# Kernel tuning notes

Measured on AMD Instinct MI355X. Metric: run time of the kernel, lower is better.

## Reference

```python
import jax, jax.numpy as jnp
import numpy as np

HIDDEN = 512

def setup_inputs() -> dict:
    key = jax.random.key(0)
    ks = jax.random.split(key, 6)
    B, T = 65536, 100
    scale = 0.1  # keep tanh MLP in a sane dynamic range
    return {
        "y0": jax.random.normal(ks[0], (B, 2), jnp.float32),
        "t_points": jnp.arange(T, dtype=jnp.float32) * 0.01,
        "W1": jax.random.normal(ks[1], (2, HIDDEN), jnp.float32) * scale,
        "b1": jnp.zeros((HIDDEN,), jnp.float32),
        "W2": jax.random.normal(ks[2], (HIDDEN, HIDDEN), jnp.float32) * scale,
        "b2": jnp.zeros((HIDDEN,), jnp.float32),
        "W3": jax.random.normal(ks[3], (HIDDEN, HIDDEN // 2), jnp.float32) * scale,
        "b3": jnp.zeros((HIDDEN // 2,), jnp.float32),
        "W4": jax.random.normal(ks[4], (HIDDEN // 2, 2), jnp.float32) * scale,
        "b4": jnp.zeros((2,), jnp.float32),
    }

def _mlp(y, W1, b1, W2, b2, W3, b3, W4, b4):
    # 4-layer tanh MLP: 2 -> H -> H -> H//2 -> 2 (t is unused in ODEFunc)
    h = jnp.tanh(y @ W1 + b1)
    h = jnp.tanh(h @ W2 + b2)
    h = jnp.tanh(h @ W3 + b3)
    return h @ W4 + b4

def reference(y0, t_points, W1, b1, W2, b2, W3, b3, W4, b4):
    f = lambda y: _mlp(y, W1, b1, W2, b2, W3, b3, W4, b4)
    dts = t_points[1:] - t_points[:-1]  # [T-1]

    def step(y, dt):
        k1 = f(y)
        k2 = f(y + k1 * (dt * 0.5))
        k3 = f(y + k2 * (dt * 0.5))
        k4 = f(y + k3 * dt)
        y_next = y + (dt / 6.0) * (k1 + 2.0 * k2 + 2.0 * k3 + k4)
        return y_next, y_next

    _, traj = jax.lax.scan(step, y0, dts)
    return jnp.concatenate([y0[None], traj], axis=0)  # [T, B, 2]
```

## Files before the change

### kernel.cpp

```cpp
#include <hip/hip_runtime.h>
#include <hip/hip_bf16.h>
#include <stdint.h>

using bfrag_t = __attribute__((ext_vector_type(8))) short;
using f32x16  = __attribute__((ext_vector_type(16))) float;

#define HID  512
#define H3   256
#define RB   128
#define NTH  512
#define KSC  2.885390081777927f

static __device__ __forceinline__ uint32_t bf16_rne(float f) {
    uint32_t u = __float_as_uint(f);
    return (u + 0x7fffu + ((u >> 16) & 1u)) >> 16;
}
static __device__ __forceinline__ uint32_t pk_bf16(float a, float b) {
    union { __hip_bfloat162 h; uint32_t u; } c;
    c.h = __float22bfloat162_rn(make_float2(a, b));
    return c.u;
}
static __device__ __forceinline__ float fast_exp2(float x) {
#if __has_builtin(__builtin_amdgcn_exp2f)
    return __builtin_amdgcn_exp2f(x);
#else
    return exp2f(x);
#endif
}
static __device__ __forceinline__ float fast_rcp(float x) {
#if __has_builtin(__builtin_amdgcn_rcpf)
    return __builtin_amdgcn_rcpf(x);
#else
    return 1.0f / x;
#endif
}
static __device__ __forceinline__ float ftanh_s(float xs) {
    float e = fast_exp2(xs);
    return 1.0f - 2.0f * fast_rcp(e + 1.0f);
}
static __device__ __forceinline__ bfrag_t frag_of(uint4 v) {
    union { uint4 u; bfrag_t f; } c; c.u = v; return c.f;
}

__global__ void prep_weights(const float* __restrict__ W1, const float* __restrict__ b1,
                             const float* __restrict__ W2, const float* __restrict__ b2,
                             const float* __restrict__ W3, const float* __restrict__ b3,
                             uint4* __restrict__ o2, uint4* __restrict__ o3,
                             float* __restrict__ w1p, float* __restrict__ b2s,
                             float* __restrict__ b3s)
{
    int id = blockIdx.x * 256 + threadIdx.x;
    if (id < 32768) {
        int l = id & 63, kt = (id >> 6) & 31, mt = id >> 11;
        int m = mt * 32 + (l & 31), k0 = kt * 16 + (l >> 5) * 8;
        uint32_t p[4];
        #pragma unroll
        for (int jj = 0; jj < 4; ++jj) {
            float v0 = KSC * W2[(k0 + jj * 2    ) * 512 + m];
            float v1 = KSC * W2[(k0 + jj * 2 + 1) * 512 + m];
            p[jj] = bf16_rne(v0) | (bf16_rne(v1) << 16);
        }
        o2[id] = make_uint4(p[0], p[1], p[2], p[3]);
    } else if (id < 49152) {
        int id2 = id - 32768;
        int l = id2 & 63, kt = (id2 >> 6) & 31, mt = id2 >> 11;
        int m = mt * 32 + (l & 31), k0 = kt * 16 + (l >> 5) * 8;
        uint32_t p[4];
        #pragma unroll
        for (int jj = 0; jj < 4; ++jj) {
            float v0 = KSC * W3[(k0 + jj * 2    ) * 256 + m];
            float v1 = KSC * W3[(k0 + jj * 2 + 1) * 256 + m];
            p[jj] = bf16_rne(v0) | (bf16_rne(v1) << 16);
        }
        o3[id2] = make_uint4(p[0], p[1], p[2], p[3]);
    } else if (id < 49152 + 1536) {
        int t = id - 49152;
        int ck = t / 24, j = t % 24;
        int f = ck * 8 + (j & 7);
        float v = (j < 8) ? W1[f] : (j < 16) ? W1[512 + f] : b1[f];
        w1p[t] = KSC * v;
    } else if (id < 49152 + 1536 + 512) {
        int i = id - 49152 - 1536; b2s[i] = KSC * b2[i];
    } else if (id < 49152 + 1536 + 512 + 256) {
        int i = id - 49152 - 1536 - 512; b3s[i] = KSC * b3[i];
    }
}

struct SmemT {
    uint4  hbuf[64 * RB];
    float  b2[HID];
    float  b3[H3];
    float  y [RB][2];
    float  z [RB][2];
    float  ya[RB][2];
    float  part[4][RB][2];
};

__global__ __launch_bounds__(NTH, 2) void node_kernel(
    const float* __restrict__ y0, const float* __restrict__ tp,
    const float* __restrict__ W4g, const float* __restrict__ b4g,
    const uint4* __restrict__ w2A, const uint4* __restrict__ w3A,
    const float* __restrict__ w1p, const float* __restrict__ b2s,
    const float* __restrict__ b3s,
    float* __restrict__ out, int Bn, int T)
{
    __shared__ SmemT s;
    const int tid = threadIdx.x;
    const int l   = tid & 63;
    const int w   = tid >> 6;
    const int wu  = __builtin_amdgcn_readfirstlane(w);
    const int b0  = blockIdx.x * RB;
    const int ln  = l & 31, lh = l >> 5;

    for (int i = tid; i < HID; i += NTH) s.b2[i] = b2s[i];
    for (int i = tid; i < H3;  i += NTH) s.b3[i] = b3s[i];
    if (tid < RB) {
        float2 v = ((const float2*)y0)[b0 + tid];
        s.y [tid][0] = v.x; s.y [tid][1] = v.y;
        s.z [tid][0] = v.x; s.z [tid][1] = v.y;
        s.ya[tid][0] = v.x; s.ya[tid][1] = v.y;
        ((float2*)out)[b0 + tid] = v;
    }
    __syncthreads();

    const float* w1w = w1p + wu * 8 * 24;
    const uint4* pW2 = w2A + (wu * 64) * 64 + l;
    const int mg = wu >> 1, ng = wu & 1;
    const uint4* pW3 = w3A + (mg * 64) * 64 + l;

    for (int st = 0; st < T - 1; ++st) {
        float dt = tp[st + 1] - tp[st];

        for (int e = 0; e < 4; ++e) {
            uint4 aC[2], aN[2];
            aC[0] = pW2[0];           aC[1] = pW2[32 * 64];
            aN[0] = pW2[64];          aN[1] = pW2[32 * 64 + 64];

            {
                float zl0 = s.z[l][0],      zl1 = s.z[l][1];
                float zh0 = s.z[64 + l][0], zh1 = s.z[64 + l][1];
                #pragma unroll
                for (int i = 0; i < 8; ++i) {
                    const float* P = w1w + i * 24;
                    int ck = wu * 8 + i;
                    float xa[8], xb[8];
                    #pragma unroll
                    for (int jj = 0; jj < 8; ++jj) {
                        float wa = P[jj], wb = P[8 + jj], bb = P[16 + jj];
                        xa[jj] = ftanh_s(fmaf(zl0, wa, fmaf(zl1, wb, bb)));
                        xb[jj] = ftanh_s(fmaf(zh0, wa, fmaf(zh1, wb, bb)));
                    }
                    s.hbuf[ck * RB + l] = make_uint4(
                        pk_bf16(xa[0], xa[1]), pk_bf16(xa[2], xa[3]),
                        pk_bf16(xa[4], xa[5]), pk_bf16(xa[6], xa[7]));
                    s.hbuf[ck * RB + 64 + l] = make_uint4(
                        pk_bf16(xb[0], xb[1]), pk_bf16(xb[2], xb[3]),
                        pk_bf16(xb[4], xb[5]), pk_bf16(xb[6], xb[7]));
                }
            }
            __syncthreads();

            uint4 a3C[2], a3N[2];
            {
                f32x16 acc[2][4];
                #pragma unroll
                for (int mt = 0; mt < 2; ++mt) {
                    int mb = (wu * 2 + mt) * 32 + 4 * lh;
                    float bv[16];
                    *(float4*)&bv[0]  = *(const float4*)&s.b2[mb];
                    *(float4*)&bv[4]  = *(const float4*)&s.b2[mb + 8];
                    *(float4*)&bv[8]  = *(const float4*)&s.b2[mb + 16];
                    *(float4*)&bv[12] = *(const float4*)&s.b2[mb + 24];
                    f32x16 a;
                    #pragma unroll
                    for (int r = 0; r < 16; ++r) a[r] = bv[r];
                    #pragma unroll
                    for (int nt = 0; nt < 4; ++nt) acc[mt][nt] = a;
                }
                #pragma unroll 2
                for (int kt = 0; kt < 32; ++kt) {
                    uint4 bF[4];
                    #pragma unroll
                    for (int nt = 0; nt < 4; ++nt)
                        bF[nt] = s.hbuf[(kt * 2 + lh) * RB + nt * 32 + ln];
                    int kq = (kt < 30) ? (kt + 2) : 29;
                    uint4 aM0 = pW2[kq * 64];
                    uint4 aM1 = pW2[32 * 64 + kq * 64];
                    #pragma unroll
                    for (int mt = 0; mt < 2; ++mt)
                        #pragma unroll
                        for (int nt = 0; nt < 4; ++nt)
                            acc[mt][nt] = __builtin_amdgcn_mfma_f32_32x32x16_bf16(
                                frag_of(aC[mt]), frag_of(bF[nt]), acc[mt][nt], 0, 0, 0);
                    aC[0] = aN[0]; aC[1] = aN[1];
                    aN[0] = aM0;   aN[1] = aM1;
                }
                a3C[0] = pW3[0];      a3C[1] = pW3[32 * 64];
                a3N[0] = pW3[64];     a3N[1] = pW3[32 * 64 + 64];
                __syncthreads();
                #pragma unroll
                for (int mt = 0; mt < 2; ++mt) {
                    int m0 = (wu * 2 + mt) * 32 + 4 * lh;
                    int hi = lh;
                    #pragma unroll
                    for (int nt = 0; nt < 4; ++nt) {
                        int n = nt * 32 + ln;
                        f32x16 c = acc[mt][nt];
                        #pragma unroll
                        for (int g = 0; g < 4; ++g) {
                            int ck = (m0 + 8 * g) >> 3;
                            uint32_t u0 = pk_bf16(ftanh_s(c[4 * g    ]), ftanh_s(c[4 * g + 1]));
                            uint32_t u1 = pk_bf16(ftanh_s(c[4 * g + 2]), ftanh_s(c[4 * g + 3]));
                            ((uint2*)s.hbuf)[((ck * RB + n) << 1) | hi] = make_uint2(u0, u1);
                        }
                    }
                }
                __syncthreads();
            }

            {
                f32x16 acc[2][2];
                #pragma unroll
                for (int mt = 0; mt < 2; ++mt) {
                    int mb = (mg * 2 + mt) * 32 + 4 * lh;
                    float bv[16];
                    *(float4*)&bv[0]  = *(const float4*)&s.b3[mb];
                    *(float4*)&bv[4]  = *(const float4*)&s.b3[mb + 8];
                    *(float4*)&bv[8]  = *(const float4*)&s.b3[mb + 16];
                    *(float4*)&bv[12] = *(const float4*)&s.b3[mb + 24];
                    f32x16 a;
                    #pragma unroll
                    for (int r = 0; r < 16; ++r) a[r] = bv[r];
                    #pragma unroll
                    for (int nt = 0; nt < 2; ++nt) acc[mt][nt] = a;
                }
                #pragma unroll 2
                for (int kt = 0; kt < 32; ++kt) {
                    uint4 bF[2];
                    #pragma unroll
                    for (int nt = 0; nt < 2; ++nt)
                        bF[nt] = s.hbuf[(kt * 2 + lh) * RB + (ng * 2 + nt) * 32 + ln];
                    int kq = (kt < 30) ? (kt + 2) : 29;
                    uint4 aM0 = pW3[kq * 64];
                    uint4 aM1 = pW3[32 * 64 + kq * 64];
                    #pragma unroll
                    for (int mt = 0; mt < 2; ++mt)
                        #pragma unroll
                        for (int nt = 0; nt < 2; ++nt)
                            acc[mt][nt] = __builtin_amdgcn_mfma_f32_32x32x16_bf16(
                                frag_of(a3C[mt]), frag_of(bF[nt]), acc[mt][nt], 0, 0, 0);
                    a3C[0] = a3N[0]; a3C[1] = a3N[1];
                    a3N[0] = aM0;    a3N[1] = aM1;
                }
                __syncthreads();
                #pragma unroll
                for (int mt = 0; mt < 2; ++mt) {
                    int m0 = (mg * 2 + mt) * 32 + 4 * lh;
                    int hi = lh;
                    #pragma unroll
                    for (int nt = 0; nt < 2; ++nt) {
                        int n = (ng * 2 + nt) * 32 + ln;
                        f32x16 c = acc[mt][nt];
                        #pragma unroll
                        for (int g = 0; g < 4; ++g) {
                            int ck = (m0 + 8 * g) >> 3;
                            uint32_t u0 = pk_bf16(ftanh_s(c[4 * g    ]), ftanh_s(c[4 * g + 1]));
                            uint32_t u1 = pk_bf16(ftanh_s(c[4 * g + 2]), ftanh_s(c[4 * g + 3]));
                            ((uint2*)s.hbuf)[((ck * RB + n) << 1) | hi] = make_uint2(u0, u1);
                        }
                    }
                }
                __syncthreads();
            }

            {
                int r  = tid & 127;
                int qq = __builtin_amdgcn_readfirstlane(tid >> 7);
                float a0 = 0.f, a1 = 0.f;
                #pragma unroll
                for (int j = 0; j < 8; ++j) {
                    int ck = qq * 8 + j;
                    uint4 hv = s.hbuf[ck * RB + r];
                    const uint32_t* pu = (const uint32_t*)&hv;
                    #pragma unroll
                    for (int jj = 0; jj < 4; ++jj) {
                        uint32_t uu = pu[jj];
                        float h0 = __uint_as_float(uu << 16);
                        float h1 = __uint_as_float(uu & 0xffff0000u);
                        int f = ck * 8 + jj * 2;
                        a0 = fmaf(h0, W4g[f * 2],     fmaf(h1, W4g[f * 2 + 2], a0));
                        a1 = fmaf(h0, W4g[f * 2 + 1], fmaf(h1, W4g[f * 2 + 3], a1));
                    }
                }
                s.part[qq][r][0] = a0; s.part[qq][r][1] = a1;
            }
            __syncthreads();

            if (tid < RB) {
                float k0 = s.part[0][tid][0] + s.part[1][tid][0]
                         + s.part[2][tid][0] + s.part[3][tid][0] + b4g[0];
                float k1 = s.part[0][tid][1] + s.part[1][tid][1]
                         + s.part[2][tid][1] + s.part[3][tid][1] + b4g[1];
                float wg = (e == 0 || e == 3) ? dt * (1.f / 6.f) : dt * (1.f / 3.f);
                float ya0 = s.ya[tid][0] + wg * k0;
                float ya1 = s.ya[tid][1] + wg * k1;
                s.ya[tid][0] = ya0; s.ya[tid][1] = ya1;
                if (e < 3) {
                    float aa = (e == 2) ? dt : dt * 0.5f;
                    s.z[tid][0] = s.y[tid][0] + aa * k0;
                    s.z[tid][1] = s.y[tid][1] + aa * k1;
                } else {
                    s.y[tid][0] = ya0; s.y[tid][1] = ya1;
                    s.z[tid][0] = ya0; s.z[tid][1] = ya1;
                    ((float2*)out)[(size_t)(st + 1) * Bn + b0 + tid] =
                        make_float2(ya0, ya1);
                }
            }
            __syncthreads();
        }
    }
}

extern "C" void kernel_launch(void* const* d_in, const int* in_sizes, int n_in,
                              void* d_out, int out_size, void* d_ws, size_t ws_size,
                              hipStream_t stream)
{
    const float* y0 = (const float*)d_in[0];
    const float* tp = (const float*)d_in[1];
    const float* W1 = (const float*)d_in[2];
    const float* b1 = (const float*)d_in[3];
    const float* W2 = (const float*)d_in[4];
    const float* b2 = (const float*)d_in[5];
    const float* W3 = (const float*)d_in[6];
    const float* b3 = (const float*)d_in[7];
    const float* W4 = (const float*)d_in[8];
    const float* b4 = (const float*)d_in[9];
    float* out = (float*)d_out;

    const int Bn = in_sizes[0] / 2;
    const int T  = in_sizes[1];

    uint4* w2A = (uint4*)d_ws;
    uint4* w3A = w2A + 32768;
    float* w1p = (float*)(w3A + 16384);
    float* b2s = w1p + 1536;
    float* b3s = b2s + 512;

    prep_weights<<<201, 256, 0, stream>>>(W1, b1, W2, b2, W3, b3,
                                          w2A, w3A, w1p, b2s, b3s);
    node_kernel<<<Bn / RB, NTH, 0, stream>>>(y0, tp, W4, b4,
                                             w2A, w3A, w1p, b2s, b3s, out, Bn, T);
}
```

Baseline: 21.86 ms.

## Halve rows per block and remap layer-3 warps to single M tiles

Each block now handles 64 batch rows instead of 128, so the grid doubles, and the launch bound asks for 4 blocks per CU instead of 2. Layer 3 is remapped so each warp owns one 32-row M tile across all N columns instead of a 2x2 M/N split. The W4 reduction is spread over 8 partial sums. The goal is more resident blocks to hide latency, but each block now reuses every global W2/W3 fragment over half as many rows, which doubles weight traffic. The tighter register budget and the 64KB-per-block LDS tile may spill registers or leave occupancy unchanged.

```diff
diff --git a/kernel.cpp b/kernel.cpp
--- a/kernel.cpp
+++ b/kernel.cpp
@@ -7,7 +7,7 @@
 
 #define HID  512
 #define H3   256
-#define RB   128
+#define RB   64
 #define NTH  512
 #define KSC  2.885390081777927f
 
@@ -93,10 +93,10 @@
     float  y [RB][2];
     float  z [RB][2];
     float  ya[RB][2];
-    float  part[4][RB][2];
+    float  part[8][RB][2];
 };
 
-__global__ __launch_bounds__(NTH, 2) void node_kernel(
+__global__ __launch_bounds__(NTH, 4) void node_kernel(
     const float* __restrict__ y0, const float* __restrict__ tp,
     const float* __restrict__ W4g, const float* __restrict__ b4g,
     const uint4* __restrict__ w2A, const uint4* __restrict__ w3A,
@@ -125,8 +125,7 @@
 
     const float* w1w = w1p + wu * 8 * 24;
     const uint4* pW2 = w2A + (wu * 64) * 64 + l;
-    const int mg = wu >> 1, ng = wu & 1;
-    const uint4* pW3 = w3A + (mg * 64) * 64 + l;
+    const uint4* pW3 = w3A + (wu * 32) * 64 + l;
 
     for (int st = 0; st < T - 1; ++st) {
         float dt = tp[st + 1] - tp[st];
@@ -137,32 +136,27 @@
             aN[0] = pW2[64];          aN[1] = pW2[32 * 64 + 64];
 
             {
-                float zl0 = s.z[l][0],      zl1 = s.z[l][1];
-                float zh0 = s.z[64 + l][0], zh1 = s.z[64 + l][1];
+                float zl0 = s.z[l][0], zl1 = s.z[l][1];
                 #pragma unroll
                 for (int i = 0; i < 8; ++i) {
                     const float* P = w1w + i * 24;
                     int ck = wu * 8 + i;
-                    float xa[8], xb[8];
+                    float xa[8];
                     #pragma unroll
                     for (int jj = 0; jj < 8; ++jj) {
                         float wa = P[jj], wb = P[8 + jj], bb = P[16 + jj];
                         xa[jj] = ftanh_s(fmaf(zl0, wa, fmaf(zl1, wb, bb)));
-                        xb[jj] = ftanh_s(fmaf(zh0, wa, fmaf(zh1, wb, bb)));
                     }
                     s.hbuf[ck * RB + l] = make_uint4(
                         pk_bf16(xa[0], xa[1]), pk_bf16(xa[2], xa[3]),
                         pk_bf16(xa[4], xa[5]), pk_bf16(xa[6], xa[7]));
-                    s.hbuf[ck * RB + 64 + l] = make_uint4(
-                        pk_bf16(xb[0], xb[1]), pk_bf16(xb[2], xb[3]),
-                        pk_bf16(xb[4], xb[5]), pk_bf16(xb[6], xb[7]));
                 }
             }
             __syncthreads();
 
-            uint4 a3C[2], a3N[2];
+            uint4 a3C, a3N;
             {
-                f32x16 acc[2][4];
+                f32x16 acc[2][2];
                 #pragma unroll
                 for (int mt = 0; mt < 2; ++mt) {
                     int mb = (wu * 2 + mt) * 32 + 4 * lh;
@@ -175,13 +169,13 @@
                     #pragma unroll
                     for (int r = 0; r < 16; ++r) a[r] = bv[r];
                     #pragma unroll
-                    for (int nt = 0; nt < 4; ++nt) acc[mt][nt] = a;
+                    for (int nt = 0; nt < 2; ++nt) acc[mt][nt] = a;
                 }
                 #pragma unroll 2
                 for (int kt = 0; kt < 32; ++kt) {
-                    uint4 bF[4];
-                    #pragma unroll
-                    for (int nt = 0; nt < 4; ++nt)
+                    uint4 bF[2];
+                    #pragma unroll
+                    for (int nt = 0; nt < 2; ++nt)
                         bF[nt] = s.hbuf[(kt * 2 + lh) * RB + nt * 32 + ln];
                     int kq = (kt < 30) ? (kt + 2) : 29;
                     uint4 aM0 = pW2[kq * 64];
@@ -189,21 +183,20 @@
                     #pragma unroll
                     for (int mt = 0; mt < 2; ++mt)
                         #pragma unroll
-                        for (int nt = 0; nt < 4; ++nt)
+                        for (int nt = 0; nt < 2; ++nt)
                             acc[mt][nt] = __builtin_amdgcn_mfma_f32_32x32x16_bf16(
                                 frag_of(aC[mt]), frag_of(bF[nt]), acc[mt][nt], 0, 0, 0);
                     aC[0] = aN[0]; aC[1] = aN[1];
                     aN[0] = aM0;   aN[1] = aM1;
                 }
-                a3C[0] = pW3[0];      a3C[1] = pW3[32 * 64];
-                a3N[0] = pW3[64];     a3N[1] = pW3[32 * 64 + 64];
+                a3C = pW3[0];      a3N = pW3[64];
                 __syncthreads();
                 #pragma unroll
                 for (int mt = 0; mt < 2; ++mt) {
                     int m0 = (wu * 2 + mt) * 32 + 4 * lh;
                     int hi = lh;
                     #pragma unroll
-                    for (int nt = 0; nt < 4; ++nt) {
+                    for (int nt = 0; nt < 2; ++nt) {
                         int n = nt * 32 + ln;
                         f32x16 c = acc[mt][nt];
                         #pragma unroll
@@ -219,10 +212,9 @@
             }
 
             {
-                f32x16 acc[2][2];
-                #pragma unroll
-                for (int mt = 0; mt < 2; ++mt) {
-                    int mb = (mg * 2 + mt) * 32 + 4 * lh;
+                f32x16 acc3[2];
+                {
+                    int mb = wu * 32 + 4 * lh;
                     float bv[16];
                     *(float4*)&bv[0]  = *(const float4*)&s.b3[mb];
                     *(float4*)&bv[4]  = *(const float4*)&s.b3[mb + 8];
@@ -231,36 +223,30 @@
                     f32x16 a;
                     #pragma unroll
                     for (int r = 0; r < 16; ++r) a[r] = bv[r];
-                    #pragma unroll
-                    for (int nt = 0; nt < 2; ++nt) acc[mt][nt] = a;
+                    acc3[0] = a; acc3[1] = a;
                 }
                 #pragma unroll 2
                 for (int kt = 0; kt < 32; ++kt) {
                     uint4 bF[2];
                     #pragma unroll
                     for (int nt = 0; nt < 2; ++nt)
-                        bF[nt] = s.hbuf[(kt * 2 + lh) * RB + (ng * 2 + nt) * 32 + ln];
+                        bF[nt] = s.hbuf[(kt * 2 + lh) * RB + nt * 32 + ln];
                     int kq = (kt < 30) ? (kt + 2) : 29;
-                    uint4 aM0 = pW3[kq * 64];
-                    uint4 aM1 = pW3[32 * 64 + kq * 64];
-                    #pragma unroll
-                    for (int mt = 0; mt < 2; ++mt)
-                        #pragma unroll
-                        for (int nt = 0; nt < 2; ++nt)
-                            acc[mt][nt] = __builtin_amdgcn_mfma_f32_32x32x16_bf16(
-                                frag_of(a3C[mt]), frag_of(bF[nt]), acc[mt][nt], 0, 0, 0);
-                    a3C[0] = a3N[0]; a3C[1] = a3N[1];
-                    a3N[0] = aM0;    a3N[1] = aM1;
+                    uint4 aM = pW3[kq * 64];
+                    #pragma unroll
+                    for (int nt = 0; nt < 2; ++nt)
+                        acc3[nt] = __builtin_amdgcn_mfma_f32_32x32x16_bf16(
+                            frag_of(a3C), frag_of(bF[nt]), acc3[nt], 0, 0, 0);
+                    a3C = a3N; a3N = aM;
                 }
                 __syncthreads();
-                #pragma unroll
-                for (int mt = 0; mt < 2; ++mt) {
-                    int m0 = (mg * 2 + mt) * 32 + 4 * lh;
+                {
+                    int m0 = wu * 32 + 4 * lh;
                     int hi = lh;
                     #pragma unroll
                     for (int nt = 0; nt < 2; ++nt) {
-                        int n = (ng * 2 + nt) * 32 + ln;
-                        f32x16 c = acc[mt][nt];
+                        int n = nt * 32 + ln;
+                        f32x16 c = acc3[nt];
                         #pragma unroll
                         for (int g = 0; g < 4; ++g) {
                             int ck = (m0 + 8 * g) >> 3;
@@ -274,12 +260,12 @@
             }
 
             {
-                int r  = tid & 127;
-                int qq = __builtin_amdgcn_readfirstlane(tid >> 7);
+                int r  = l;
+                int qq = wu;
                 float a0 = 0.f, a1 = 0.f;
                 #pragma unroll
-                for (int j = 0; j < 8; ++j) {
-                    int ck = qq * 8 + j;
+                for (int j = 0; j < 4; ++j) {
+                    int ck = qq * 4 + j;
                     uint4 hv = s.hbuf[ck * RB + r];
                     const uint32_t* pu = (const uint32_t*)&hv;
                     #pragma unroll
@@ -297,10 +283,12 @@
             __syncthreads();
 
             if (tid < RB) {
-                float k0 = s.part[0][tid][0] + s.part[1][tid][0]
-                         + s.part[2][tid][0] + s.part[3][tid][0] + b4g[0];
-                float k1 = s.part[0][tid][1] + s.part[1][tid][1]
-                         + s.part[2][tid][1] + s.part[3][tid][1] + b4g[1];
+                float k0 = b4g[0], k1 = b4g[1];
+                #pragma unroll
+                for (int p = 0; p < 8; ++p) {
+                    k0 += s.part[p][tid][0];
+                    k1 += s.part[p][tid][1];
+                }
                 float wg = (e == 0 || e == 3) ? dt * (1.f / 6.f) : dt * (1.f / 3.f);
                 float ya0 = s.ya[tid][0] + wg * k0;
                 float ya1 = s.ya[tid][1] + wg * k1;
```

Measured after the change: 26.77 ms. 1.22x slower.

## Fuse layer-4 projection into layer-3 MFMA epilogue, drop hbuf round trip

Applied to the files above, without the earlier changes.

The final 256->2 projection is now computed directly from the layer-3 MFMA accumulators in registers, using a W4 copy permuted to the accumulator layout in the prep kernel. Per-wave partial sums go to an 8-way partial buffer that is reduced per row. This removes the bf16 tanh writeback to shared memory, one barrier, and the separate reduction pass that re-read hbuf. It also keeps layer-3 activations in fp32 rather than bf16 for the last layer. The cost is a larger reduction and more scalar weight loads per lane.

```diff
diff --git a/kernel.cpp b/kernel.cpp
--- a/kernel.cpp
+++ b/kernel.cpp
@@ -45,9 +45,10 @@
 __global__ void prep_weights(const float* __restrict__ W1, const float* __restrict__ b1,
                              const float* __restrict__ W2, const float* __restrict__ b2,
                              const float* __restrict__ W3, const float* __restrict__ b3,
+                             const float* __restrict__ W4,
                              uint4* __restrict__ o2, uint4* __restrict__ o3,
                              float* __restrict__ w1p, float* __restrict__ b2s,
-                             float* __restrict__ b3s)
+                             float* __restrict__ b3s, float* __restrict__ w4f)
 {
     int id = blockIdx.x * 256 + threadIdx.x;
     if (id < 32768) {
@@ -83,6 +84,15 @@
         int i = id - 49152 - 1536; b2s[i] = KSC * b2[i];
     } else if (id < 49152 + 1536 + 512 + 256) {
         int i = id - 49152 - 1536 - 512; b3s[i] = KSC * b3[i];
+    } else if (id < 49152 + 1536 + 512 + 256 + 512) {
+        int t = id - (49152 + 1536 + 512 + 256);
+        int c  = t & 1;
+        int rg = (t >> 1) & 15;
+        int mt = (t >> 5) & 1;
+        int lh = (t >> 6) & 1;
+        int mg = (t >> 7) & 3;
+        int m = (mg * 2 + mt) * 32 + (rg & 3) + 8 * (rg >> 2) + 4 * lh;
+        w4f[t] = W4[m * 2 + c];
     }
 }
 
@@ -93,12 +103,12 @@
     float  y [RB][2];
     float  z [RB][2];
     float  ya[RB][2];
-    float  part[4][RB][2];
+    float  part[8][RB][2];
 };
 
 __global__ __launch_bounds__(NTH, 2) void node_kernel(
     const float* __restrict__ y0, const float* __restrict__ tp,
-    const float* __restrict__ W4g, const float* __restrict__ b4g,
+    const float* __restrict__ w4f, const float* __restrict__ b4g,
     const uint4* __restrict__ w2A, const uint4* __restrict__ w3A,
     const float* __restrict__ w1p, const float* __restrict__ b2s,
     const float* __restrict__ b3s,
@@ -111,6 +121,7 @@
     const int wu  = __builtin_amdgcn_readfirstlane(w);
     const int b0  = blockIdx.x * RB;
     const int ln  = l & 31, lh = l >> 5;
+    const int mg  = wu >> 1, ng = wu & 1;
 
     for (int i = tid; i < HID; i += NTH) s.b2[i] = b2s[i];
     for (int i = tid; i < H3;  i += NTH) s.b3[i] = b3s[i];
@@ -125,16 +136,16 @@
 
     const float* w1w = w1p + wu * 8 * 24;
     const uint4* pW2 = w2A + (wu * 64) * 64 + l;
-    const int mg = wu >> 1, ng = wu & 1;
     const uint4* pW3 = w3A + (mg * 64) * 64 + l;
+    const float* w4w = w4f + (mg * 2 + lh) * 64;
 
     for (int st = 0; st < T - 1; ++st) {
         float dt = tp[st + 1] - tp[st];
 
         for (int e = 0; e < 4; ++e) {
             uint4 aC[2], aN[2];
-            aC[0] = pW2[0];           aC[1] = pW2[32 * 64];
-            aN[0] = pW2[64];          aN[1] = pW2[32 * 64 + 64];
+            aC[0] = pW2[0];           aC[1] = pW2[2048];
+            aN[0] = pW2[64];          aN[1] = pW2[2048 + 64];
 
             {
                 float zl0 = s.z[l][0],      zl1 = s.z[l][1];
@@ -185,7 +196,7 @@
                         bF[nt] = s.hbuf[(kt * 2 + lh) * RB + nt * 32 + ln];
                     int kq = (kt < 30) ? (kt + 2) : 29;
                     uint4 aM0 = pW2[kq * 64];
-                    uint4 aM1 = pW2[32 * 64 + kq * 64];
+                    uint4 aM1 = pW2[2048 + kq * 64];
                     #pragma unroll
                     for (int mt = 0; mt < 2; ++mt)
                         #pragma unroll
@@ -195,8 +206,8 @@
                     aC[0] = aN[0]; aC[1] = aN[1];
                     aN[0] = aM0;   aN[1] = aM1;
                 }
-                a3C[0] = pW3[0];      a3C[1] = pW3[32 * 64];
-                a3N[0] = pW3[64];     a3N[1] = pW3[32 * 64 + 64];
+                a3C[0] = pW3[0];      a3C[1] = pW3[2048];
+                a3N[0] = pW3[64];     a3N[1] = pW3[2048 + 64];
                 __syncthreads();
                 #pragma unroll
                 for (int mt = 0; mt < 2; ++mt) {
@@ -219,7 +230,7 @@
             }
 
             {
-                f32x16 acc[2][2];
+                f32x16 acc3[2][2];
                 #pragma unroll
                 for (int mt = 0; mt < 2; ++mt) {
                     int mb = (mg * 2 + mt) * 32 + 4 * lh;
@@ -232,75 +243,52 @@
                     #pragma unroll
                     for (int r = 0; r < 16; ++r) a[r] = bv[r];
                     #pragma unroll
-                    for (int nt = 0; nt < 2; ++nt) acc[mt][nt] = a;
+                    for (int nt = 0; nt < 2; ++nt) acc3[mt][nt] = a;
                 }
                 #pragma unroll 2
                 for (int kt = 0; kt < 32; ++kt) {
                     uint4 bF[2];
                     #pragma unroll
                     for (int nt = 0; nt < 2; ++nt)
-                        bF[nt] = s.hbuf[(kt * 2 + lh) * RB + (ng * 2 + nt) * 32 + ln];
+                        bF[nt] = s.hbuf[(kt * 2 + lh) * RB + ng * 64 + nt * 32 + ln];
                     int kq = (kt < 30) ? (kt + 2) : 29;
                     uint4 aM0 = pW3[kq * 64];
-                    uint4 aM1 = pW3[32 * 64 + kq * 64];
+                    uint4 aM1 = pW3[2048 + kq * 64];
                     #pragma unroll
                     for (int mt = 0; mt < 2; ++mt)
                         #pragma unroll
                         for (int nt = 0; nt < 2; ++nt)
-                            acc[mt][nt] = __builtin_amdgcn_mfma_f32_32x32x16_bf16(
-                                frag_of(a3C[mt]), frag_of(bF[nt]), acc[mt][nt], 0, 0, 0);
+                            acc3[mt][nt] = __builtin_amdgcn_mfma_f32_32x32x16_bf16(
+                                frag_of(a3C[mt]), frag_of(bF[nt]), acc3[mt][nt], 0, 0, 0);
                     a3C[0] = a3N[0]; a3C[1] = a3N[1];
                     a3N[0] = aM0;    a3N[1] = aM1;
                 }
-                __syncthreads();
-                #pragma unroll
-                for (int mt = 0; mt < 2; ++mt) {
-                    int m0 = (mg * 2 + mt) * 32 + 4 * lh;
-                    int hi = lh;
-                    #pragma unroll
-                    for (int nt = 0; nt < 2; ++nt) {
-                        int n = (ng * 2 + nt) * 32 + ln;
-                        f32x16 c = acc[mt][nt];
-                        #pragma unroll
-                        for (int g = 0; g < 4; ++g) {
-                            int ck = (m0 + 8 * g) >> 3;
-                            uint32_t u0 = pk_bf16(ftanh_s(c[4 * g    ]), ftanh_s(c[4 * g + 1]));
-                            uint32_t u1 = pk_bf16(ftanh_s(c[4 * g + 2]), ftanh_s(c[4 * g + 3]));
-                            ((uint2*)s.hbuf)[((ck * RB + n) << 1) | hi] = make_uint2(u0, u1);
-                        }
+                float pk00 = 0.f, pk01 = 0.f, pk10 = 0.f, pk11 = 0.f;
+                #pragma unroll
+                for (int mt = 0; mt < 2; ++mt)
+                    #pragma unroll
+                    for (int r = 0; r < 16; ++r) {
+                        float wp0 = w4w[mt * 32 + r * 2];
+                        float wp1 = w4w[mt * 32 + r * 2 + 1];
+                        float h0 = ftanh_s(acc3[mt][0][r]);
+                        float h1 = ftanh_s(acc3[mt][1][r]);
+                        pk00 = fmaf(h0, wp0, pk00); pk01 = fmaf(h0, wp1, pk01);
+                        pk10 = fmaf(h1, wp0, pk10); pk11 = fmaf(h1, wp1, pk11);
                     }
-                }
-                __syncthreads();
-            }
-
-            {
-                int r  = tid & 127;
-                int qq = __builtin_amdgcn_readfirstlane(tid >> 7);
-                float a0 = 0.f, a1 = 0.f;
-                #pragma unroll
-                for (int j = 0; j < 8; ++j) {
-                    int ck = qq * 8 + j;
-                    uint4 hv = s.hbuf[ck * RB + r];
-                    const uint32_t* pu = (const uint32_t*)&hv;
-                    #pragma unroll
-                    for (int jj = 0; jj < 4; ++jj) {
-                        uint32_t uu = pu[jj];
-                        float h0 = __uint_as_float(uu << 16);
-                        float h1 = __uint_as_float(uu & 0xffff0000u);
-                        int f = ck * 8 + jj * 2;
-                        a0 = fmaf(h0, W4g[f * 2],     fmaf(h1, W4g[f * 2 + 2], a0));
-                        a1 = fmaf(h0, W4g[f * 2 + 1], fmaf(h1, W4g[f * 2 + 3], a1));
-                    }
-                }
-                s.part[qq][r][0] = a0; s.part[qq][r][1] = a1;
+                int n0 = ng * 64 + ln;
+                int pi = mg * 2 + lh;
+                s.part[pi][n0][0]      = pk00; s.part[pi][n0][1]      = pk01;
+                s.part[pi][n0 + 32][0] = pk10; s.part[pi][n0 + 32][1] = pk11;
             }
             __syncthreads();
 
             if (tid < RB) {
-                float k0 = s.part[0][tid][0] + s.part[1][tid][0]
-                         + s.part[2][tid][0] + s.part[3][tid][0] + b4g[0];
-                float k1 = s.part[0][tid][1] + s.part[1][tid][1]
-                         + s.part[2][tid][1] + s.part[3][tid][1] + b4g[1];
+                float k0 = b4g[0], k1 = b4g[1];
+                #pragma unroll
+                for (int p = 0; p < 8; ++p) {
+                    k0 += s.part[p][tid][0];
+                    k1 += s.part[p][tid][1];
+                }
                 float wg = (e == 0 || e == 3) ? dt * (1.f / 6.f) : dt * (1.f / 3.f);
                 float ya0 = s.ya[tid][0] + wg * k0;
                 float ya1 = s.ya[tid][1] + wg * k1;
@@ -345,9 +333,10 @@
     float* w1p = (float*)(w3A + 16384);
     float* b2s = w1p + 1536;
     float* b3s = b2s + 512;
-
-    prep_weights<<<201, 256, 0, stream>>>(W1, b1, W2, b2, W3, b3,
-                                          w2A, w3A, w1p, b2s, b3s);
-    node_kernel<<<Bn / RB, NTH, 0, stream>>>(y0, tp, W4, b4,
+    float* w4f = b3s + 256;
+
+    prep_weights<<<203, 256, 0, stream>>>(W1, b1, W2, b2, W3, b3, W4,
+                                          w2A, w3A, w1p, b2s, b3s, w4f);
+    node_kernel<<<Bn / RB, NTH, 0, stream>>>(y0, tp, w4f, b4,
                                              w2A, w3A, w1p, b2s, b3s, out, Bn, T);
 }
```

Measured after the change: 25.42 ms. +16.3%, slower.
